# Optimization experiments

Measured on AMD Instinct MI355X. Metric: run time of the kernel, lower is better.

Reference implementation:

```python
import jax, jax.numpy as jnp
import numpy as np

LOG2 = float(np.log(2.0))

def ssp(x):
    # shifted softplus: softplus(x) - log(2)
    return jax.nn.softplus(x) - LOG2

def setup_inputs() -> dict:
    key = jax.random.key(0)
    ks = jax.random.split(key, 16)
    N, E, F = 50000, 800000, 128  # atoms, interactions, feature/filter dim
    s = 0.05
    return {
        "x": jax.random.normal(ks[0], (N, F), jnp.float32),
        "dijk": jax.random.uniform(ks[1], (E, F), jnp.float32),
        "idx_j": jax.random.randint(ks[2], (E,), 0, N),
        "seg_i": jnp.sort(jax.random.randint(ks[3], (E,), 0, N)),
        "seg_j": jnp.arange(E),
        "seg_i_sum": N,
        "W1": jax.random.normal(ks[4], (F, F), jnp.float32) * s,
        "b1": jnp.zeros((F,), jnp.float32),
        "W2": jax.random.normal(ks[5], (F, F), jnp.float32) * s,
        "b2": jnp.zeros((F,), jnp.float32),
        "W_in2fac": jax.random.normal(ks[6], (F, F), jnp.float32) * s,
        "W_fac2out": jax.random.normal(ks[7], (F, F), jnp.float32) * s,
        "b_fac2out": jnp.zeros((F,), jnp.float32),
        "W_dense": jax.random.normal(ks[8], (F, F), jnp.float32) * s,
        "b_dense": jnp.zeros((F,), jnp.float32),
    }

def reference(x, dijk, idx_j, seg_i, seg_j, seg_i_sum,
              W1, b1, W2, b2, W_in2fac, W_fac2out, b_fac2out, W_dense, b_dense):
    E = dijk.shape[0]
    # --- CFnetFilter: dense -> dense -> segment-sum over seg_j ---
    h = ssp(dijk @ W1 + b1)                        # [E, F]
    w_ijk = ssp(h @ W2 + b2)                       # [E, F]
    w_ij = jax.ops.segment_sum(w_ijk, seg_j, num_segments=E)  # [E, F]
    # --- CFConv: in2fac -> gather idx_j -> filter mult -> segment-sum seg_i -> fac2out ---
    f = x @ W_in2fac                               # [N, F]
    f = f[idx_j]                                   # gather, [E, F]
    wf = w_ij * f                                  # [E, F]
    conv = jax.ops.segment_sum(wf, seg_i, num_segments=seg_i_sum)  # [N, F]
    c = ssp(conv @ W_fac2out + b_fac2out)          # [N, F]
    # --- residual dense ---
    v = c @ W_dense + b_dense                      # [N, F]
    y = x + v
    return (y, v)
```

## Files before the change

kernel.cpp:

```cpp
#include <hip/hip_runtime.h>
#include <hip/hip_bf16.h>

#define F 128

typedef __attribute__((ext_vector_type(8))) short bf16x8;
typedef __attribute__((ext_vector_type(4))) float f32x4;


__device__ __forceinline__ short f2bf(float f) {
  union { float f; unsigned u; } v; v.f = f;
  unsigned r = (v.u + 0x7FFFu + ((v.u >> 16) & 1u)) >> 16;
  return (short)r;
}

__device__ __forceinline__ float sspf(float x) {
  float t = __expf(-fabsf(x));
  return fmaxf(x, 0.0f) + __logf(1.0f + t) - 0.69314718055994530942f;
}

__device__ __forceinline__ int h_idx(int row, int k) {
  int chunk = k >> 3;
  int sw = chunk ^ (row & 15);
  return row * 128 + sw * 8 + (k & 7);
}

__device__ __forceinline__ int wf_idx(int row, int c) {
  return row * 128 + (c ^ ((row & 4) << 2));
}

__device__ __forceinline__ bf16x8 load_bfrag(const short* sW, int nt, int kb, int lane) {
  return *(const bf16x8*)(sW + (((nt * 4 + kb) * 64 + lane) << 3));
}

__device__ __forceinline__ bf16x8 load_afrag_f32(const float* __restrict__ p, bool valid) {
  bf16x8 a = {0, 0, 0, 0, 0, 0, 0, 0};
  if (valid) {
    const float4* q = (const float4*)p;
    float4 x0 = q[0], x1 = q[1];
    a[0] = f2bf(x0.x); a[1] = f2bf(x0.y); a[2] = f2bf(x0.z); a[3] = f2bf(x0.w);
    a[4] = f2bf(x1.x); a[5] = f2bf(x1.y); a[6] = f2bf(x1.z); a[7] = f2bf(x1.w);
  }
  return a;
}

__global__ void prep_weights(const float* __restrict__ W1, const float* __restrict__ W2,
                             const float* __restrict__ Wi2f, const float* __restrict__ Wf2o,
                             const float* __restrict__ Wd, unsigned short* __restrict__ out) {
  int t = blockIdx.x * 256 + threadIdx.x;
  int m = t >> 14;
  int idx = t & 16383;
  int k = idx >> 7, n = idx & 127;
  const float* W = (m == 0) ? W1 : (m == 1) ? W2 : (m == 2) ? Wi2f : (m == 3) ? Wf2o : Wd;
  float v = W[idx];
  int nt = n >> 4, kb = k >> 5;
  int lane = (((k >> 3) & 3) << 4) | (n & 15);
  int j = k & 7;
  int dst = (((nt * 4 + kb) * 64 + lane) << 3) | j;
  out[(m << 14) + dst] = (unsigned short)f2bf(v);
}

__global__ __launch_bounds__(256, 2) void f_kernel(const float* __restrict__ x,
                                                   const unsigned short* __restrict__ wfrag,
                                                   float* __restrict__ f, int N) {
  __shared__ union { short s[16384]; float4 v4[2048]; } sm;
  const int tid = threadIdx.x;
  const int lane = tid & 63, wv = tid >> 6;
  const int quad = lane >> 4, ln = lane & 15;
  const int r0 = blockIdx.x * 128;

  {
    const float4* src = (const float4*)(wfrag + 2 * 16384);
#pragma unroll
    for (int i = 0; i < 8; ++i) sm.v4[tid + 256 * i] = src[tid + 256 * i];
  }

  bf16x8 a1[2][4];
#pragma unroll
  for (int mt = 0; mt < 2; ++mt) {
    int row = r0 + wv * 32 + mt * 16 + ln;
    bool valid = row < N;
    const float* rp = x + (size_t)row * F + quad * 8;
#pragma unroll
    for (int kb = 0; kb < 4; ++kb) a1[mt][kb] = load_afrag_f32(rp + kb * 32, valid);
  }
  __syncthreads();

#pragma unroll
  for (int nt = 0; nt < 8; ++nt) {
    f32x4 acc0 = {0, 0, 0, 0}, acc1 = {0, 0, 0, 0};
#pragma unroll
    for (int kb = 0; kb < 4; ++kb) {
      bf16x8 b = load_bfrag(sm.s, nt, kb, lane);
      acc0 = __builtin_amdgcn_mfma_f32_16x16x32_bf16(a1[0][kb], b, acc0, 0, 0, 0);
      acc1 = __builtin_amdgcn_mfma_f32_16x16x32_bf16(a1[1][kb], b, acc1, 0, 0, 0);
    }
    int col = nt * 16 + ln;
#pragma unroll
    for (int mt = 0; mt < 2; ++mt) {
#pragma unroll
      for (int r = 0; r < 4; ++r) {
        int row = r0 + wv * 32 + mt * 16 + quad * 4 + r;
        if (row < N) f[(size_t)row * F + col] = (mt == 0) ? acc0[r] : acc1[r];
      }
    }
  }
}

__global__ __launch_bounds__(256, 2) void edge_kernel(
    const float* __restrict__ dijk, const int* __restrict__ idx_j, const int* __restrict__ seg_i,
    const float* __restrict__ b1, const float* __restrict__ b2,
    const unsigned short* __restrict__ wfrag, const float* __restrict__ f,
    float* __restrict__ conv, int E) {
  __shared__ union { short s[32768]; float fl[16384]; float4 v4[4096]; } sm;
  __shared__ int sIdx[128];
  __shared__ int sSeg[128];

  const int tid = threadIdx.x;
  const int lane = tid & 63, wv = tid >> 6;
  const int quad = lane >> 4, ln = lane & 15;
  const int e0 = blockIdx.x * 128;

  {
    const float4* src = (const float4*)wfrag;
#pragma unroll
    for (int i = 0; i < 16; ++i) sm.v4[tid + 256 * i] = src[tid + 256 * i];
  }
  if (tid < 128) {
    int e = e0 + tid;
    sIdx[tid] = (e < E) ? idx_j[e] : 0;
    sSeg[tid] = (e < E) ? seg_i[e] : -1;
  }

  float bias1v[8], bias2v[8];
#pragma unroll
  for (int nt = 0; nt < 8; ++nt) {
    bias1v[nt] = b1[nt * 16 + ln];
    bias2v[nt] = b2[nt * 16 + ln];
  }

  bf16x8 a1[2][4];
#pragma unroll
  for (int mt = 0; mt < 2; ++mt) {
    int row = e0 + wv * 32 + mt * 16 + ln;
    bool valid = row < E;
    const float* rp = dijk + (size_t)row * F + quad * 8;
#pragma unroll
    for (int kb = 0; kb < 4; ++kb) a1[mt][kb] = load_afrag_f32(rp + kb * 32, valid);
  }
  __syncthreads();

  short hreg[2][8][4];
  const short* sW1 = sm.s;
  const short* sW2 = sm.s + 16384;
#pragma unroll
  for (int nt = 0; nt < 8; ++nt) {
    f32x4 acc0 = {0, 0, 0, 0}, acc1 = {0, 0, 0, 0};
#pragma unroll
    for (int kb = 0; kb < 4; ++kb) {
      bf16x8 b = load_bfrag(sW1, nt, kb, lane);
      acc0 = __builtin_amdgcn_mfma_f32_16x16x32_bf16(a1[0][kb], b, acc0, 0, 0, 0);
      acc1 = __builtin_amdgcn_mfma_f32_16x16x32_bf16(a1[1][kb], b, acc1, 0, 0, 0);
    }
#pragma unroll
    for (int r = 0; r < 4; ++r) {
      hreg[0][nt][r] = f2bf(sspf(acc0[r] + bias1v[nt]));
      hreg[1][nt][r] = f2bf(sspf(acc1[r] + bias1v[nt]));
    }
  }
  __syncthreads();

  short* sH = sm.s;
#pragma unroll
  for (int mt = 0; mt < 2; ++mt)
#pragma unroll
    for (int nt = 0; nt < 8; ++nt)
#pragma unroll
      for (int r = 0; r < 4; ++r) {
        int row = wv * 32 + mt * 16 + quad * 4 + r;
        sH[h_idx(row, nt * 16 + ln)] = hreg[mt][nt][r];
      }
  __syncthreads();

  bf16x8 a2[2][4];
#pragma unroll
  for (int mt = 0; mt < 2; ++mt) {
    int row = wv * 32 + mt * 16 + ln;
#pragma unroll
    for (int kb = 0; kb < 4; ++kb)
      a2[mt][kb] = *(const bf16x8*)(sH + h_idx(row, kb * 32 + quad * 8));
  }

  float wreg[2][8][4];
#pragma unroll
  for (int nt = 0; nt < 8; ++nt) {
    f32x4 acc0 = {0, 0, 0, 0}, acc1 = {0, 0, 0, 0};
#pragma unroll
    for (int kb = 0; kb < 4; ++kb) {
      bf16x8 b = load_bfrag(sW2, nt, kb, lane);
      acc0 = __builtin_amdgcn_mfma_f32_16x16x32_bf16(a2[0][kb], b, acc0, 0, 0, 0);
      acc1 = __builtin_amdgcn_mfma_f32_16x16x32_bf16(a2[1][kb], b, acc1, 0, 0, 0);
    }
#pragma unroll
    for (int r = 0; r < 4; ++r) {
      wreg[0][nt][r] = sspf(acc0[r] + bias2v[nt]);
      wreg[1][nt][r] = sspf(acc1[r] + bias2v[nt]);
    }
  }
  __syncthreads();

  float* sWF = sm.fl;
#pragma unroll
  for (int mt = 0; mt < 2; ++mt)
#pragma unroll
    for (int r = 0; r < 4; ++r) {
      int rloc = wv * 32 + mt * 16 + quad * 4 + r;
      int jrow = sIdx[rloc];
      const float* fp = f + (size_t)jrow * F;
#pragma unroll
      for (int nt = 0; nt < 8; ++nt) {
        int c = nt * 16 + ln;
        sWF[wf_idx(rloc, c)] = wreg[mt][nt][r] * fp[c];
      }
    }
  __syncthreads();

  {
    int c = tid & 127;
    int half = tid >> 7;
    int r0 = half * 64;
    float acc = 0.0f;
    int cur = sSeg[r0];
    for (int r = r0; r < r0 + 64; ++r) {
      int s = sSeg[r];
      if (s != cur) {
        if (cur >= 0) atomicAdd(conv + (size_t)cur * F + c, acc);
        acc = 0.0f; cur = s;
      }
      acc += sWF[wf_idx(r, c)];
    }
    if (cur >= 0) atomicAdd(conv + (size_t)cur * F + c, acc);
  }
}

__global__ __launch_bounds__(256, 2) void node_kernel(
    const float* __restrict__ conv, const float* __restrict__ x,
    const float* __restrict__ bf2o, const float* __restrict__ bd,
    const unsigned short* __restrict__ wfrag, float* __restrict__ y,
    float* __restrict__ vout, int N) {
  __shared__ union { short s[32768]; float4 v4[4096]; } sm;
  const int tid = threadIdx.x;
  const int lane = tid & 63, wv = tid >> 6;
  const int quad = lane >> 4, ln = lane & 15;
  const int r0 = blockIdx.x * 128;

  {
    const float4* src = (const float4*)(wfrag + 3 * 16384);
#pragma unroll
    for (int i = 0; i < 16; ++i) sm.v4[tid + 256 * i] = src[tid + 256 * i];
  }

  float bfv[8], bdv[8];
#pragma unroll
  for (int nt = 0; nt < 8; ++nt) {
    bfv[nt] = bf2o[nt * 16 + ln];
    bdv[nt] = bd[nt * 16 + ln];
  }

  bf16x8 a1[2][4];
#pragma unroll
  for (int mt = 0; mt < 2; ++mt) {
    int row = r0 + wv * 32 + mt * 16 + ln;
    bool valid = row < N;
    const float* rp = conv + (size_t)row * F + quad * 8;
#pragma unroll
    for (int kb = 0; kb < 4; ++kb) a1[mt][kb] = load_afrag_f32(rp + kb * 32, valid);
  }
  __syncthreads();

  short creg[2][8][4];
  const short* sWa = sm.s;
  const short* sWd = sm.s + 16384;
#pragma unroll
  for (int nt = 0; nt < 8; ++nt) {
    f32x4 acc0 = {0, 0, 0, 0}, acc1 = {0, 0, 0, 0};
#pragma unroll
    for (int kb = 0; kb < 4; ++kb) {
      bf16x8 b = load_bfrag(sWa, nt, kb, lane);
      acc0 = __builtin_amdgcn_mfma_f32_16x16x32_bf16(a1[0][kb], b, acc0, 0, 0, 0);
      acc1 = __builtin_amdgcn_mfma_f32_16x16x32_bf16(a1[1][kb], b, acc1, 0, 0, 0);
    }
#pragma unroll
    for (int r = 0; r < 4; ++r) {
      creg[0][nt][r] = f2bf(sspf(acc0[r] + bfv[nt]));
      creg[1][nt][r] = f2bf(sspf(acc1[r] + bfv[nt]));
    }
  }
  __syncthreads();

  short* sC = sm.s;
#pragma unroll
  for (int mt = 0; mt < 2; ++mt)
#pragma unroll
    for (int nt = 0; nt < 8; ++nt)
#pragma unroll
      for (int r = 0; r < 4; ++r) {
        int row = wv * 32 + mt * 16 + quad * 4 + r;
        sC[h_idx(row, nt * 16 + ln)] = creg[mt][nt][r];
      }
  __syncthreads();

  bf16x8 a2[2][4];
#pragma unroll
  for (int mt = 0; mt < 2; ++mt) {
    int row = wv * 32 + mt * 16 + ln;
#pragma unroll
    for (int kb = 0; kb < 4; ++kb)
      a2[mt][kb] = *(const bf16x8*)(sC + h_idx(row, kb * 32 + quad * 8));
  }

#pragma unroll
  for (int nt = 0; nt < 8; ++nt) {
    f32x4 acc0 = {0, 0, 0, 0}, acc1 = {0, 0, 0, 0};
#pragma unroll
    for (int kb = 0; kb < 4; ++kb) {
      bf16x8 b = load_bfrag(sWd, nt, kb, lane);
      acc0 = __builtin_amdgcn_mfma_f32_16x16x32_bf16(a2[0][kb], b, acc0, 0, 0, 0);
      acc1 = __builtin_amdgcn_mfma_f32_16x16x32_bf16(a2[1][kb], b, acc1, 0, 0, 0);
    }
    int col = nt * 16 + ln;
#pragma unroll
    for (int mt = 0; mt < 2; ++mt) {
#pragma unroll
      for (int r = 0; r < 4; ++r) {
        int row = r0 + wv * 32 + mt * 16 + quad * 4 + r;
        if (row < N) {
          float v = ((mt == 0) ? acc0[r] : acc1[r]) + bdv[nt];
          size_t o = (size_t)row * F + col;
          y[o] = x[o] + v;
          vout[o] = v;
        }
      }
    }
  }
}

extern "C" void kernel_launch(void* const* d_in, const int* in_sizes, int n_in,
                              void* d_out, int out_size, void* d_ws, size_t ws_size,
                              hipStream_t stream) {
  const float* x    = (const float*)d_in[0];
  const float* dijk = (const float*)d_in[1];
  const int*   idxj = (const int*)d_in[2];
  const int*   segi = (const int*)d_in[3];
  const float* W1   = (const float*)d_in[6];
  const float* b1   = (const float*)d_in[7];
  const float* W2   = (const float*)d_in[8];
  const float* b2   = (const float*)d_in[9];
  const float* Wi2f = (const float*)d_in[10];
  const float* Wf2o = (const float*)d_in[11];
  const float* bf2o = (const float*)d_in[12];
  const float* Wd   = (const float*)d_in[13];
  const float* bd   = (const float*)d_in[14];

  int N = in_sizes[0] / F;
  int E = in_sizes[1] / F;

  unsigned short* wfrag = (unsigned short*)d_ws;
  float* fbuf = (float*)((char*)d_ws + 5 * 16384 * sizeof(unsigned short));
  float* conv = fbuf + (size_t)N * F;

  float* y = (float*)d_out;
  float* vout = y + (size_t)N * F;

  hipMemsetAsync(conv, 0, (size_t)N * F * sizeof(float), stream);
  prep_weights<<<320, 256, 0, stream>>>(W1, W2, Wi2f, Wf2o, Wd, wfrag);

  int nb = (N + 127) / 128;
  int eb = (E + 127) / 128;
  f_kernel<<<nb, 256, 0, stream>>>(x, wfrag, fbuf, N);
  edge_kernel<<<eb, 256, 0, stream>>>(dijk, idxj, segi, b1, b2, wfrag, fbuf, conv, E);
  node_kernel<<<nb, 256, 0, stream>>>(conv, x, bf2o, bd, wfrag, y, vout, N);
}
```

Before: 842.3 us.

## Read weight fragments from global memory, shrink LDS, restructure edge gather-reduce

Weight B-fragments are now loaded straight from global memory (served by the cache) instead of being staged into LDS, so every kernel drops its weight-copy prologue and LDS use falls to 32 KB, allowing occupancy 4 in the launch bounds. In the edge kernel, the second-layer output is written back into the shared h buffer as bf16, and the gather-multiply is fused into the segment reduction: each thread handles 4 columns over 16 rows using float4 gathers of f. Float-to-bf16 conversion uses the packed intrinsic. This adds an extra rounding of w_ij to bf16, more atomics per block because the segment runs are shorter (16 rows instead of 64), and repeated global or L2 weight reads per wave.

Result: slower. 889.3 us (+5.6%).

```diff
diff --git a/kernel.cpp b/kernel.cpp
--- a/kernel.cpp
+++ b/kernel.cpp
@@ -13,6 +13,17 @@
   return (short)r;
 }
 
+__device__ __forceinline__ float bf2f(short s) {
+  union { unsigned u; float f; } v;
+  v.u = ((unsigned)(unsigned short)s) << 16;
+  return v.f;
+}
+
+__device__ __forceinline__ short2 pk2(float a, float b) {
+  __hip_bfloat162 p = __float22bfloat162_rn(make_float2(a, b));
+  union { __hip_bfloat162 h; short2 s; } u; u.h = p; return u.s;
+}
+
 __device__ __forceinline__ float sspf(float x) {
   float t = __expf(-fabsf(x));
   return fmaxf(x, 0.0f) + __logf(1.0f + t) - 0.69314718055994530942f;
@@ -24,12 +35,9 @@
   return row * 128 + sw * 8 + (k & 7);
 }
 
-__device__ __forceinline__ int wf_idx(int row, int c) {
-  return row * 128 + (c ^ ((row & 4) << 2));
-}
-
-__device__ __forceinline__ bf16x8 load_bfrag(const short* sW, int nt, int kb, int lane) {
-  return *(const bf16x8*)(sW + (((nt * 4 + kb) * 64 + lane) << 3));
+__device__ __forceinline__ bf16x8 load_bfrag_g(const unsigned short* __restrict__ W,
+                                               int nt, int kb, int lane) {
+  return *(const bf16x8*)(W + (((nt * 4 + kb) * 64 + lane) << 3));
 }
 
 __device__ __forceinline__ bf16x8 load_afrag_f32(const float* __restrict__ p, bool valid) {
@@ -37,8 +45,10 @@
   if (valid) {
     const float4* q = (const float4*)p;
     float4 x0 = q[0], x1 = q[1];
-    a[0] = f2bf(x0.x); a[1] = f2bf(x0.y); a[2] = f2bf(x0.z); a[3] = f2bf(x0.w);
-    a[4] = f2bf(x1.x); a[5] = f2bf(x1.y); a[6] = f2bf(x1.z); a[7] = f2bf(x1.w);
+    short2 p0 = pk2(x0.x, x0.y), p1 = pk2(x0.z, x0.w);
+    short2 p2 = pk2(x1.x, x1.y), p3 = pk2(x1.z, x1.w);
+    a[0] = p0.x; a[1] = p0.y; a[2] = p1.x; a[3] = p1.y;
+    a[4] = p2.x; a[5] = p2.y; a[6] = p3.x; a[7] = p3.y;
   }
   return a;
 }
@@ -59,20 +69,14 @@
   out[(m << 14) + dst] = (unsigned short)f2bf(v);
 }
 
-__global__ __launch_bounds__(256, 2) void f_kernel(const float* __restrict__ x,
+__global__ __launch_bounds__(256, 4) void f_kernel(const float* __restrict__ x,
                                                    const unsigned short* __restrict__ wfrag,
                                                    float* __restrict__ f, int N) {
-  __shared__ union { short s[16384]; float4 v4[2048]; } sm;
   const int tid = threadIdx.x;
   const int lane = tid & 63, wv = tid >> 6;
   const int quad = lane >> 4, ln = lane & 15;
   const int r0 = blockIdx.x * 128;
-
-  {
-    const float4* src = (const float4*)(wfrag + 2 * 16384);
-#pragma unroll
-    for (int i = 0; i < 8; ++i) sm.v4[tid + 256 * i] = src[tid + 256 * i];
-  }
+  const unsigned short* gW = wfrag + 2 * 16384;
 
   bf16x8 a1[2][4];
 #pragma unroll
@@ -83,14 +87,13 @@
 #pragma unroll
     for (int kb = 0; kb < 4; ++kb) a1[mt][kb] = load_afrag_f32(rp + kb * 32, valid);
   }
-  __syncthreads();
-
-#pragma unroll
-  for (int nt = 0; nt < 8; ++nt) {
-    f32x4 acc0 = {0, 0, 0, 0}, acc1 = {0, 0, 0, 0};
-#pragma unroll
-    for (int kb = 0; kb < 4; ++kb) {
-      bf16x8 b = load_bfrag(sm.s, nt, kb, lane);
+
+#pragma unroll
+  for (int nt = 0; nt < 8; ++nt) {
+    f32x4 acc0 = {0, 0, 0, 0}, acc1 = {0, 0, 0, 0};
+#pragma unroll
+    for (int kb = 0; kb < 4; ++kb) {
+      bf16x8 b = load_bfrag_g(gW, nt, kb, lane);
       acc0 = __builtin_amdgcn_mfma_f32_16x16x32_bf16(a1[0][kb], b, acc0, 0, 0, 0);
       acc1 = __builtin_amdgcn_mfma_f32_16x16x32_bf16(a1[1][kb], b, acc1, 0, 0, 0);
     }
@@ -106,12 +109,12 @@
   }
 }
 
-__global__ __launch_bounds__(256, 2) void edge_kernel(
+__global__ __launch_bounds__(256, 4) void edge_kernel(
     const float* __restrict__ dijk, const int* __restrict__ idx_j, const int* __restrict__ seg_i,
     const float* __restrict__ b1, const float* __restrict__ b2,
     const unsigned short* __restrict__ wfrag, const float* __restrict__ f,
     float* __restrict__ conv, int E) {
-  __shared__ union { short s[32768]; float fl[16384]; float4 v4[4096]; } sm;
+  __shared__ short sH[16384];
   __shared__ int sIdx[128];
   __shared__ int sSeg[128];
 
@@ -119,12 +122,9 @@
   const int lane = tid & 63, wv = tid >> 6;
   const int quad = lane >> 4, ln = lane & 15;
   const int e0 = blockIdx.x * 128;
-
-  {
-    const float4* src = (const float4*)wfrag;
-#pragma unroll
-    for (int i = 0; i < 16; ++i) sm.v4[tid + 256 * i] = src[tid + 256 * i];
-  }
+  const unsigned short* gW1 = wfrag;
+  const unsigned short* gW2 = wfrag + 16384;
+
   if (tid < 128) {
     int e = e0 + tid;
     sIdx[tid] = (e < E) ? idx_j[e] : 0;
@@ -147,38 +147,23 @@
 #pragma unroll
     for (int kb = 0; kb < 4; ++kb) a1[mt][kb] = load_afrag_f32(rp + kb * 32, valid);
   }
-  __syncthreads();
-
-  short hreg[2][8][4];
-  const short* sW1 = sm.s;
-  const short* sW2 = sm.s + 16384;
-#pragma unroll
-  for (int nt = 0; nt < 8; ++nt) {
-    f32x4 acc0 = {0, 0, 0, 0}, acc1 = {0, 0, 0, 0};
-#pragma unroll
-    for (int kb = 0; kb < 4; ++kb) {
-      bf16x8 b = load_bfrag(sW1, nt, kb, lane);
+
+#pragma unroll
+  for (int nt = 0; nt < 8; ++nt) {
+    f32x4 acc0 = {0, 0, 0, 0}, acc1 = {0, 0, 0, 0};
+#pragma unroll
+    for (int kb = 0; kb < 4; ++kb) {
+      bf16x8 b = load_bfrag_g(gW1, nt, kb, lane);
       acc0 = __builtin_amdgcn_mfma_f32_16x16x32_bf16(a1[0][kb], b, acc0, 0, 0, 0);
       acc1 = __builtin_amdgcn_mfma_f32_16x16x32_bf16(a1[1][kb], b, acc1, 0, 0, 0);
     }
+    int col = nt * 16 + ln;
 #pragma unroll
     for (int r = 0; r < 4; ++r) {
-      hreg[0][nt][r] = f2bf(sspf(acc0[r] + bias1v[nt]));
-      hreg[1][nt][r] = f2bf(sspf(acc1[r] + bias1v[nt]));
-    }
-  }
-  __syncthreads();
-
-  short* sH = sm.s;
-#pragma unroll
-  for (int mt = 0; mt < 2; ++mt)
-#pragma unroll
-    for (int nt = 0; nt < 8; ++nt)
-#pragma unroll
-      for (int r = 0; r < 4; ++r) {
-        int row = wv * 32 + mt * 16 + quad * 4 + r;
-        sH[h_idx(row, nt * 16 + ln)] = hreg[mt][nt][r];
-      }
+      sH[h_idx(wv * 32 + quad * 4 + r, col)] = f2bf(sspf(acc0[r] + bias1v[nt]));
+      sH[h_idx(wv * 32 + 16 + quad * 4 + r, col)] = f2bf(sspf(acc1[r] + bias1v[nt]));
+    }
+  }
   __syncthreads();
 
   bf16x8 a2[2][4];
@@ -189,75 +174,72 @@
     for (int kb = 0; kb < 4; ++kb)
       a2[mt][kb] = *(const bf16x8*)(sH + h_idx(row, kb * 32 + quad * 8));
   }
-
-  float wreg[2][8][4];
-#pragma unroll
-  for (int nt = 0; nt < 8; ++nt) {
-    f32x4 acc0 = {0, 0, 0, 0}, acc1 = {0, 0, 0, 0};
-#pragma unroll
-    for (int kb = 0; kb < 4; ++kb) {
-      bf16x8 b = load_bfrag(sW2, nt, kb, lane);
+  __syncthreads();
+
+#pragma unroll
+  for (int nt = 0; nt < 8; ++nt) {
+    f32x4 acc0 = {0, 0, 0, 0}, acc1 = {0, 0, 0, 0};
+#pragma unroll
+    for (int kb = 0; kb < 4; ++kb) {
+      bf16x8 b = load_bfrag_g(gW2, nt, kb, lane);
       acc0 = __builtin_amdgcn_mfma_f32_16x16x32_bf16(a2[0][kb], b, acc0, 0, 0, 0);
       acc1 = __builtin_amdgcn_mfma_f32_16x16x32_bf16(a2[1][kb], b, acc1, 0, 0, 0);
     }
+    int col = nt * 16 + ln;
 #pragma unroll
     for (int r = 0; r < 4; ++r) {
-      wreg[0][nt][r] = sspf(acc0[r] + bias2v[nt]);
-      wreg[1][nt][r] = sspf(acc1[r] + bias2v[nt]);
+      sH[h_idx(wv * 32 + quad * 4 + r, col)] = f2bf(sspf(acc0[r] + bias2v[nt]));
+      sH[h_idx(wv * 32 + 16 + quad * 4 + r, col)] = f2bf(sspf(acc1[r] + bias2v[nt]));
     }
   }
   __syncthreads();
 
-  float* sWF = sm.fl;
-#pragma unroll
-  for (int mt = 0; mt < 2; ++mt)
-#pragma unroll
-    for (int r = 0; r < 4; ++r) {
-      int rloc = wv * 32 + mt * 16 + quad * 4 + r;
-      int jrow = sIdx[rloc];
-      const float* fp = f + (size_t)jrow * F;
-#pragma unroll
-      for (int nt = 0; nt < 8; ++nt) {
-        int c = nt * 16 + ln;
-        sWF[wf_idx(rloc, c)] = wreg[mt][nt][r] * fp[c];
-      }
-    }
-  __syncthreads();
-
   {
-    int c = tid & 127;
-    int half = tid >> 7;
-    int r0 = half * 64;
-    float acc = 0.0f;
-    int cur = sSeg[r0];
-    for (int r = r0; r < r0 + 64; ++r) {
+    const int cg = tid & 31;
+    const int r0l = (tid >> 5) * 16;
+    const int c0 = cg * 4;
+    f32x4 acc = {0, 0, 0, 0};
+    int cur = sSeg[r0l];
+    for (int r = r0l; r < r0l + 16; ++r) {
       int s = sSeg[r];
       if (s != cur) {
-        if (cur >= 0) atomicAdd(conv + (size_t)cur * F + c, acc);
-        acc = 0.0f; cur = s;
+        if (cur >= 0) {
+          float* p = conv + (size_t)cur * F + c0;
+          atomicAdd(p + 0, acc[0]); atomicAdd(p + 1, acc[1]);
+          atomicAdd(p + 2, acc[2]); atomicAdd(p + 3, acc[3]);
+        }
+        acc[0] = acc[1] = acc[2] = acc[3] = 0.0f;
+        cur = s;
       }
-      acc += sWF[wf_idx(r, c)];
-    }
-    if (cur >= 0) atomicAdd(conv + (size_t)cur * F + c, acc);
-  }
-}
-
-__global__ __launch_bounds__(256, 2) void node_kernel(
+      int jrow = sIdx[r];
+      int off = r * 128 + ((((c0 >> 3) ^ (r & 15)) << 3)) + (c0 & 7);
+      short4 w = *(const short4*)(sH + off);
+      float4 fv = *(const float4*)(f + (size_t)jrow * F + c0);
+      acc[0] = fmaf(bf2f(w.x), fv.x, acc[0]);
+      acc[1] = fmaf(bf2f(w.y), fv.y, acc[1]);
+      acc[2] = fmaf(bf2f(w.z), fv.z, acc[2]);
+      acc[3] = fmaf(bf2f(w.w), fv.w, acc[3]);
+    }
+    if (cur >= 0) {
+      float* p = conv + (size_t)cur * F + c0;
+      atomicAdd(p + 0, acc[0]); atomicAdd(p + 1, acc[1]);
+      atomicAdd(p + 2, acc[2]); atomicAdd(p + 3, acc[3]);
+    }
+  }
+}
+
+__global__ __launch_bounds__(256, 4) void node_kernel(
     const float* __restrict__ conv, const float* __restrict__ x,
     const float* __restrict__ bf2o, const float* __restrict__ bd,
     const unsigned short* __restrict__ wfrag, float* __restrict__ y,
     float* __restrict__ vout, int N) {
-  __shared__ union { short s[32768]; float4 v4[4096]; } sm;
+  __shared__ short sC[16384];
   const int tid = threadIdx.x;
   const int lane = tid & 63, wv = tid >> 6;
   const int quad = lane >> 4, ln = lane & 15;
   const int r0 = blockIdx.x * 128;
-
-  {
-    const float4* src = (const float4*)(wfrag + 3 * 16384);
-#pragma unroll
-    for (int i = 0; i < 16; ++i) sm.v4[tid + 256 * i] = src[tid + 256 * i];
-  }
+  const unsigned short* gWa = wfrag + 3 * 16384;
+  const unsigned short* gWd = wfrag + 4 * 16384;
 
   float bfv[8], bdv[8];
 #pragma unroll
@@ -275,38 +257,23 @@
 #pragma unroll
     for (int kb = 0; kb < 4; ++kb) a1[mt][kb] = load_afrag_f32(rp + kb * 32, valid);
   }
-  __syncthreads();
-
-  short creg[2][8][4];
-  const short* sWa = sm.s;
-  const short* sWd = sm.s + 16384;
-#pragma unroll
-  for (int nt = 0; nt < 8; ++nt) {
-    f32x4 acc0 = {0, 0, 0, 0}, acc1 = {0, 0, 0, 0};
-#pragma unroll
-    for (int kb = 0; kb < 4; ++kb) {
-      bf16x8 b = load_bfrag(sWa, nt, kb, lane);
+
+#pragma unroll
+  for (int nt = 0; nt < 8; ++nt) {
+    f32x4 acc0 = {0, 0, 0, 0}, acc1 = {0, 0, 0, 0};
+#pragma unroll
+    for (int kb = 0; kb < 4; ++kb) {
+      bf16x8 b = load_bfrag_g(gWa, nt, kb, lane);
       acc0 = __builtin_amdgcn_mfma_f32_16x16x32_bf16(a1[0][kb], b, acc0, 0, 0, 0);
       acc1 = __builtin_amdgcn_mfma_f32_16x16x32_bf16(a1[1][kb], b, acc1, 0, 0, 0);
     }
+    int col = nt * 16 + ln;
 #pragma unroll
     for (int r = 0; r < 4; ++r) {
-      creg[0][nt][r] = f2bf(sspf(acc0[r] + bfv[nt]));
-      creg[1][nt][r] = f2bf(sspf(acc1[r] + bfv[nt]));
-    }
-  }
-  __syncthreads();
-
-  short* sC = sm.s;
-#pragma unroll
-  for (int mt = 0; mt < 2; ++mt)
-#pragma unroll
-    for (int nt = 0; nt < 8; ++nt)
-#pragma unroll
-      for (int r = 0; r < 4; ++r) {
-        int row = wv * 32 + mt * 16 + quad * 4 + r;
-        sC[h_idx(row, nt * 16 + ln)] = creg[mt][nt][r];
-      }
+      sC[h_idx(wv * 32 + quad * 4 + r, col)] = f2bf(sspf(acc0[r] + bfv[nt]));
+      sC[h_idx(wv * 32 + 16 + quad * 4 + r, col)] = f2bf(sspf(acc1[r] + bfv[nt]));
+    }
+  }
   __syncthreads();
 
   bf16x8 a2[2][4];
@@ -323,7 +290,7 @@
     f32x4 acc0 = {0, 0, 0, 0}, acc1 = {0, 0, 0, 0};
 #pragma unroll
     for (int kb = 0; kb < 4; ++kb) {
-      bf16x8 b = load_bfrag(sWd, nt, kb, lane);
+      bf16x8 b = load_bfrag_g(gWd, nt, kb, lane);
       acc0 = __builtin_amdgcn_mfma_f32_16x16x32_bf16(a2[0][kb], b, acc0, 0, 0, 0);
       acc1 = __builtin_amdgcn_mfma_f32_16x16x32_bf16(a2[1][kb], b, acc1, 0, 0, 0);
     }
```
